# Kernel tuning notes

Measured on AMD Instinct MI355X. Metric: run time of the kernel, lower is better.

Reference implementation:

```python
import jax, jax.numpy as jnp
import numpy as np

# ---- Kymatio-style Morlet scattering filter bank (J=2, L=8, padded 40x40) ----
_CACHE = {}
_MP = 40  # 32 + 2*4 reflect padding, as in kymatio compute_padding for J=2

def _gabor(M, N, sigma, theta, xi, slant):
    R = np.array([[np.cos(theta), -np.sin(theta)], [np.sin(theta), np.cos(theta)]])
    D = np.array([[1.0, 0.0], [0.0, slant ** 2]])
    curv = R @ D @ R.T / (2.0 * sigma ** 2)
    xx, yy = np.mgrid[0:M, 0:N]
    gab = np.zeros((M, N), np.complex128)
    for ex in range(-2, 3):  # periodize over 5x5 shifts
        for ey in range(-2, 3):
            xg = xx + ex * M
            yg = yy + ey * N
            arg = -(curv[0, 0] * xg * xg + (curv[0, 1] + curv[1, 0]) * xg * yg + curv[1, 1] * yg * yg) \
                  + 1j * (xg * xi * np.cos(theta) + yg * xi * np.sin(theta))
            gab += np.exp(arg)
    return gab / (2.0 * np.pi * sigma ** 2 / slant)

def _morlet(M, N, sigma, theta, xi, slant):
    wv = _gabor(M, N, sigma, theta, xi, slant)
    env = _gabor(M, N, sigma, theta, 0.0, slant)
    return wv - (wv.sum() / env.sum()) * env  # zero-mean Morlet

def _periodize(v, res):
    k = 2 ** res
    Mv, Nv = v.shape
    return v.reshape(k, Mv // k, k, Nv // k).mean(axis=(0, 2))

def _filters():
    if _CACHE:
        return _CACHE
    Mp = _MP
    phi = np.real(np.fft.fft2(_gabor(Mp, Mp, 0.8 * 2 ** 2, 0.0, 0.0, 1.0)))
    psis = {}
    for j in range(2):
        bank = []
        for t in range(8):
            theta = (3 - t) * np.pi / 8.0  # kymatio angle convention (L=8)
            bank.append(np.real(np.fft.fft2(_morlet(Mp, Mp, 0.8 * 2 ** j, theta, 3.0 * np.pi / 4.0 / 2 ** j, 0.5))))
        psis[j] = np.stack(bank)
    _CACHE['phi0'] = jnp.asarray(phi, jnp.float32)
    _CACHE['phi1'] = jnp.asarray(_periodize(phi, 1), jnp.float32)
    _CACHE['psi0'] = jnp.asarray(psis[0], jnp.float32)      # (8,40,40) j=0 at res 0
    _CACHE['psi1_r0'] = jnp.asarray(psis[1], jnp.float32)   # (8,40,40) j=1 at res 0
    return _CACHE

def _unpad_sub(y_real, k):
    # fourier lowpass output -> spatial subsample by k, then unpad 1-pixel border
    return y_real[..., ::k, ::k][..., 1:-1, 1:-1]

def _scatter(x):
    F = _filters()
    xp = jnp.pad(x, ((0, 0), (0, 0), (4, 4), (4, 4)), mode='reflect')  # (B,3,40,40)
    xf = jnp.fft.fft2(xp)
    def lowpass(u, phi, k):
        return _unpad_sub(jnp.fft.ifft2(jnp.fft.fft2(u) * phi).real, k)
    # order 0
    S0 = _unpad_sub(jnp.fft.ifft2(xf * F['phi0']).real, 4)[:, :, None]            # (B,3,1,8,8)
    # order 1, j1 = 0 (stays at res 0)
    U1a = jnp.abs(jnp.fft.ifft2(xf[:, :, None] * F['psi0']))                       # (B,3,8,40,40)
    S1a = lowpass(U1a, F['phi0'], 4)                                               # (B,3,8,8,8)
    # order 1, j1 = 1 (subsample by 2)
    U1b = jnp.abs(jnp.fft.ifft2(xf[:, :, None] * F['psi1_r0'])[..., ::2, ::2])     # (B,3,8,20,20)
    S1b = lowpass(U1b, F['phi1'], 2)                                               # (B,3,8,8,8)
    # order 2, j1=0 -> j2=1
    U2 = jnp.abs(jnp.fft.ifft2(jnp.fft.fft2(U1a)[:, :, :, None] * F['psi1_r0'])[..., ::2, ::2])  # (B,3,8,8,20,20)
    S2 = lowpass(U2, F['phi1'], 2).reshape(x.shape[0], 3, 64, 8, 8)
    return jnp.concatenate([S0, S1a, S1b, S2], axis=2)  # (B,3,81,8,8)

def _toeplitz_mult(G, H, v):
    # ToeplitzLike, corner=False -> f=(0,0): y = sum_i L(g_i) (L(h_i)^T v)
    # L(.) lower-triangular Toeplitz; done via length-2n FFT conv / correlation
    n = v.shape[-1]
    Lf = 2 * n
    Hf = jnp.fft.rfft(H, Lf)          # (r, F)
    Gf = jnp.fft.rfft(G, Lf)          # (r, F)
    Vf = jnp.fft.rfft(v, Lf)          # (B, F)
    T = jnp.fft.irfft(jnp.conj(Hf)[:, None, :] * Vf[None], Lf)[..., :n]   # (r,B,n) = L(h_i)^T v
    Tf = jnp.fft.rfft(T, Lf)
    y = jnp.fft.irfft(jnp.einsum('rf,rbf->bf', Gf, Tf), Lf)[..., :n]       # sum_i L(g_i) t_i
    return y

def setup_inputs() -> dict:
    key = jax.random.key(0)
    ks = jax.random.split(key, 5)
    B, n, r = 128, 3 * 81 * 8 * 8, 4
    x = jax.random.normal(ks[0], (B, 3, 32, 32), jnp.float32)
    gamma = jnp.ones((n,), jnp.float32)
    beta = jnp.zeros((n,), jnp.float32)
    G = jax.random.normal(ks[3], (r, n), jnp.float32) / np.float32(np.sqrt(n))
    H = jax.random.normal(ks[4], (r, n), jnp.float32) / np.float32(np.sqrt(n))
    return {"x": x, "gamma": gamma, "beta": beta, "G": G, "H": H}

def reference(x, gamma, beta, G, H):
    S = _scatter(x)                                   # (B,3,81,8,8)
    f = S.reshape(S.shape[0], -1)                     # (B, 15552)
    mu = f.mean(axis=0)
    var = f.var(axis=0)                               # biased var, training-mode BN
    f = (f - mu) / jnp.sqrt(var + 1e-5) * gamma + beta
    f = jax.nn.relu(f)
    y = _toeplitz_mult(G, H, f)
    return y[..., :10]
```

## Files before the change

### kernel.cpp

```cpp
#include <hip/hip_runtime.h>
#include <math.h>

#define NTHR 256

__device__ __forceinline__ int reflect32(int v) {
  if (v < 0) v = -v;
  if (v > 31) v = 62 - v;
  return v;
}

__device__ __forceinline__ void init_tw(float2* tw, int N, int tid) {
  for (int j = tid; j < N; j += NTHR) {
    float s, c;
    sincosf(-2.0f * (float)M_PI * (float)j / (float)N, &s, &c);
    tw[j] = make_float2(c, s);
  }
}

template<int N, int LD, int NK, bool INV, int B, int AS>
__device__ __forceinline__ void dftB_rows(const float2* __restrict__ io,
                                          float2* __restrict__ tmp,
                                          const float2* __restrict__ tw, int tid) {
  constexpr int G = N / NK;
  constexpr int UNITS = B * N * G;
  for (int u = tid; u < UNITS; u += NTHR) {
    const int a = u / (N * G);
    const int rem = u - a * (N * G);
    const int r = rem / G, kg = rem - G * r;
    float xr[NK], xi[NK], ar[NK], ai[NK];
#pragma unroll
    for (int j = 0; j < NK; ++j) {
      float2 w = tw[kg * NK + j];
      xr[j] = w.x; xi[j] = INV ? -w.y : w.y;
    }
    const float2* row = io + a * AS + r * LD;
    float2 v = row[N - 1];
#pragma unroll
    for (int j = 0; j < NK; ++j) { ar[j] = v.x; ai[j] = v.y; }
#pragma unroll 2
    for (int cc = N - 2; cc >= 0; --cc) {
      v = row[cc];
#pragma unroll
      for (int j = 0; j < NK; ++j) {
        float nr = fmaf(ar[j], xr[j], fmaf(-ai[j], xi[j], v.x));
        float ni = fmaf(ar[j], xi[j], fmaf(ai[j], xr[j], v.y));
        ar[j] = nr; ai[j] = ni;
      }
    }
    float2* orow = tmp + a * AS + r * LD + kg * NK;
#pragma unroll
    for (int j = 0; j < NK; ++j) orow[j] = make_float2(ar[j], ai[j]);
  }
}

template<int N, int LD, int NK, bool INV, int B, int AS>
__device__ __forceinline__ void dftB_cols(const float2* __restrict__ tmp,
                                          float2* __restrict__ io,
                                          const float2* __restrict__ tw, int tid) {
  constexpr int G = N / NK;
  constexpr int UNITS = B * N * G;
  for (int u = tid; u < UNITS; u += NTHR) {
    const int a = u / (N * G);
    const int rem = u - a * (N * G);
    const int k1g = rem / N, k2 = rem - N * k1g;
    float xr[NK], xi[NK], ar[NK], ai[NK];
#pragma unroll
    for (int j = 0; j < NK; ++j) {
      float2 w = tw[k1g * NK + j];
      xr[j] = w.x; xi[j] = INV ? -w.y : w.y;
    }
    const float2* col = tmp + a * AS + k2;
    float2 v = col[(N - 1) * LD];
#pragma unroll
    for (int j = 0; j < NK; ++j) { ar[j] = v.x; ai[j] = v.y; }
#pragma unroll 2
    for (int r = N - 2; r >= 0; --r) {
      v = col[r * LD];
#pragma unroll
      for (int j = 0; j < NK; ++j) {
        float nr = fmaf(ar[j], xr[j], fmaf(-ai[j], xi[j], v.x));
        float ni = fmaf(ar[j], xi[j], fmaf(ai[j], xr[j], v.y));
        ar[j] = nr; ai[j] = ni;
      }
    }
    constexpr float scale = INV ? (1.f / (float)(N * N)) : 1.f;
#pragma unroll
    for (int j = 0; j < NK; ++j)
      io[a * AS + (k1g * NK + j) * LD + k2] = make_float2(ar[j] * scale, ai[j] * scale);
  }
}

template<int N, int LD, int NK, bool INV, int B, int AS>
__device__ __forceinline__ void dft2dB(float2* io, float2* tmp, const float2* tw, int tid) {
  dftB_rows<N, LD, NK, INV, B, AS>(io, tmp, tw, tid);
  __syncthreads();
  dftB_cols<N, LD, NK, INV, B, AS>(tmp, io, tw, tid);
  __syncthreads();
}

template<bool INV>
__device__ __forceinline__ void r40_rowsA(const float2* __restrict__ io, float2* __restrict__ T,
                                          const float2* __restrict__ tw, int tid) {
  if (tid < 200) {
    const int r = tid / 5, n2 = tid - 5 * r;
    const float2* base = io + r * 41 + n2;
    float xr[8], xi[8], ar[8], ai[8];
#pragma unroll
    for (int k1 = 0; k1 < 8; ++k1) {
      float2 w = tw[5 * k1];
      xr[k1] = w.x; xi[k1] = INV ? -w.y : w.y;
    }
    float2 v = base[35];
#pragma unroll
    for (int k1 = 0; k1 < 8; ++k1) { ar[k1] = v.x; ai[k1] = v.y; }
#pragma unroll
    for (int n1 = 6; n1 >= 0; --n1) {
      v = base[5 * n1];
#pragma unroll
      for (int k1 = 0; k1 < 8; ++k1) {
        float nr = fmaf(ar[k1], xr[k1], fmaf(-ai[k1], xi[k1], v.x));
        float ni = fmaf(ar[k1], xi[k1], fmaf(ai[k1], xr[k1], v.y));
        ar[k1] = nr; ai[k1] = ni;
      }
    }
    float2* o = T + r * 41 + n2 * 8;
#pragma unroll
    for (int k1 = 0; k1 < 8; ++k1) {
      float2 w = tw[n2 * k1];
      float wy = INV ? -w.y : w.y;
      o[k1] = make_float2(ar[k1] * w.x - ai[k1] * wy, ar[k1] * wy + ai[k1] * w.x);
    }
  }
}

template<bool INV>
__device__ __forceinline__ void r40_rowsB(const float2* __restrict__ T, float2* __restrict__ io,
                                          const float2* __restrict__ tw, int tid) {
  for (int u = tid; u < 320; u += NTHR) {
    const int r = u >> 3, k1 = u & 7;
    const float2* base = T + r * 41 + k1;
    float xr[5], xi[5], ar[5], ai[5];
#pragma unroll
    for (int k2 = 0; k2 < 5; ++k2) {
      float2 w = tw[8 * k2];
      xr[k2] = w.x; xi[k2] = INV ? -w.y : w.y;
    }
    float2 v = base[32];
#pragma unroll
    for (int k2 = 0; k2 < 5; ++k2) { ar[k2] = v.x; ai[k2] = v.y; }
#pragma unroll
    for (int n2 = 3; n2 >= 0; --n2) {
      v = base[n2 * 8];
#pragma unroll
      for (int k2 = 0; k2 < 5; ++k2) {
        float nr = fmaf(ar[k2], xr[k2], fmaf(-ai[k2], xi[k2], v.x));
        float ni = fmaf(ar[k2], xi[k2], fmaf(ai[k2], xr[k2], v.y));
        ar[k2] = nr; ai[k2] = ni;
      }
    }
    float2* o = io + r * 41 + k1;
#pragma unroll
    for (int k2 = 0; k2 < 5; ++k2) o[8 * k2] = make_float2(ar[k2], ai[k2]);
  }
}

template<bool INV>
__device__ __forceinline__ void r40_colsA(const float2* __restrict__ io, float2* __restrict__ T,
                                          const float2* __restrict__ tw, int tid) {
  if (tid < 200) {
    const int n2 = tid / 40, c = tid - 40 * n2;
    const float2* base = io + n2 * 41 + c;
    float xr[8], xi[8], ar[8], ai[8];
#pragma unroll
    for (int k1 = 0; k1 < 8; ++k1) {
      float2 w = tw[5 * k1];
      xr[k1] = w.x; xi[k1] = INV ? -w.y : w.y;
    }
    float2 v = base[35 * 41];
#pragma unroll
    for (int k1 = 0; k1 < 8; ++k1) { ar[k1] = v.x; ai[k1] = v.y; }
#pragma unroll
    for (int n1 = 6; n1 >= 0; --n1) {
      v = base[5 * n1 * 41];
#pragma unroll
      for (int k1 = 0; k1 < 8; ++k1) {
        float nr = fmaf(ar[k1], xr[k1], fmaf(-ai[k1], xi[k1], v.x));
        float ni = fmaf(ar[k1], xi[k1], fmaf(ai[k1], xr[k1], v.y));
        ar[k1] = nr; ai[k1] = ni;
      }
    }
    float2* o = T + n2 * 8 * 41 + c;
#pragma unroll
    for (int k1 = 0; k1 < 8; ++k1) {
      float2 w = tw[n2 * k1];
      float wy = INV ? -w.y : w.y;
      o[k1 * 41] = make_float2(ar[k1] * w.x - ai[k1] * wy, ar[k1] * wy + ai[k1] * w.x);
    }
  }
}

template<bool INV>
__device__ __forceinline__ void r40_colsB(const float2* __restrict__ T, float2* __restrict__ io,
                                          const float2* __restrict__ tw, int tid) {
  constexpr float scale = INV ? (1.f / 1600.f) : 1.f;
  for (int u = tid; u < 320; u += NTHR) {
    const int k1 = u / 40, c = u - 40 * k1;
    const float2* base = T + k1 * 41 + c;
    float xr[5], xi[5], ar[5], ai[5];
#pragma unroll
    for (int k2 = 0; k2 < 5; ++k2) {
      float2 w = tw[8 * k2];
      xr[k2] = w.x; xi[k2] = INV ? -w.y : w.y;
    }
    float2 v = base[4 * 8 * 41];
#pragma unroll
    for (int k2 = 0; k2 < 5; ++k2) { ar[k2] = v.x; ai[k2] = v.y; }
#pragma unroll
    for (int n2 = 3; n2 >= 0; --n2) {
      v = base[n2 * 8 * 41];
#pragma unroll
      for (int k2 = 0; k2 < 5; ++k2) {
        float nr = fmaf(ar[k2], xr[k2], fmaf(-ai[k2], xi[k2], v.x));
        float ni = fmaf(ar[k2], xi[k2], fmaf(ai[k2], xr[k2], v.y));
        ar[k2] = nr; ai[k2] = ni;
      }
    }
    float2* o = io + k1 * 41 + c;
#pragma unroll
    for (int k2 = 0; k2 < 5; ++k2)
      o[8 * k2 * 41] = make_float2(ar[k2] * scale, ai[k2] * scale);
  }
}

template<bool INV>
__device__ __forceinline__ void radix40(float2* io, float2* T, const float2* tw, int tid) {
  r40_rowsA<INV>(io, T, tw, tid);
  __syncthreads();
  r40_rowsB<INV>(T, io, tw, tid);
  __syncthreads();
  r40_colsA<INV>(io, T, tw, tid);
  __syncthreads();
  r40_colsB<INV>(T, io, tw, tid);
  __syncthreads();
}

__global__ __launch_bounds__(NTHR) void k_filters(float* __restrict__ filt) {
  const int fid = blockIdx.x;
  const int tid = threadIdx.x;

  __shared__ float2 WV[40 * 41];
  __shared__ float  EV[1600];
  __shared__ float2 T[40 * 41];
  __shared__ float2 tw40[40];
  __shared__ float  sred[3][4];
  __shared__ float  Kc[2];

  double sigma, theta, xi, slant; int morlet;
  if (fid == 0)      { sigma = 3.2; theta = 0.0; xi = 0.0;                  slant = 1.0; morlet = 0; }
  else if (fid <= 8) { int t = fid - 1; sigma = 0.8; theta = (3 - t) * M_PI / 8.0; xi = 3.0 * M_PI / 4.0; slant = 0.5; morlet = 1; }
  else               { int t = fid - 9; sigma = 1.6; theta = (3 - t) * M_PI / 8.0; xi = 3.0 * M_PI / 8.0; slant = 0.5; morlet = 1; }

  const double ctd = cos(theta), std_ = sin(theta);
  const double sl2 = slant * slant;
  const double inv2s = 1.0 / (2.0 * sigma * sigma);
  const float ca = (float)((ctd * ctd + sl2 * std_ * std_) * inv2s);
  const float cb = (float)((ctd * std_ * (1.0 - sl2)) * inv2s);
  const float cd = (float)((std_ * std_ + sl2 * ctd * ctd) * inv2s);
  const float rnorm = (float)(slant / (2.0 * M_PI * sigma * sigma));
  const float ct = (float)ctd, st = (float)std_;
  const float xif = (float)xi;

  float swr = 0.f, swi = 0.f, ser = 0.f;
  for (int o = tid; o < 1600; o += NTHR) {
    int xr = o / 40, yc = o - 40 * xr;
    float wr = 0.f, wi = 0.f, er = 0.f;
    for (int ex = -2; ex <= 2; ++ex) {
      for (int ey = -2; ey <= 2; ++ey) {
        float xg = (float)xr + ex * 40.f, yg = (float)yc + ey * 40.f;
        float e = expf(-(ca * xg * xg + 2.f * cb * xg * yg + cd * yg * yg));
        float ang = xif * (xg * ct + yg * st);
        float s, c;
        sincosf(ang, &s, &c);
        wr = fmaf(e, c, wr); wi = fmaf(e, s, wi); er += e;
      }
    }
    wr *= rnorm; wi *= rnorm; er *= rnorm;
    WV[xr * 41 + yc] = make_float2(wr, wi);
    EV[o] = er;
    swr += wr; swi += wi; ser += er;
  }
  for (int off = 32; off > 0; off >>= 1) {
    swr += __shfl_down(swr, off);
    swi += __shfl_down(swi, off);
    ser += __shfl_down(ser, off);
  }
  int lane = tid & 63, w = tid >> 6;
  if (lane == 0) { sred[0][w] = swr; sred[1][w] = swi; sred[2][w] = ser; }
  __syncthreads();
  if (tid == 0) {
    float A = 0, B = 0, C = 0;
    for (int i = 0; i < 4; ++i) { A += sred[0][i]; B += sred[1][i]; C += sred[2][i]; }
    Kc[0] = A / C; Kc[1] = B / C;
  }
  init_tw(tw40, 40, tid);
  __syncthreads();
  if (morlet) {
    for (int o = tid; o < 1600; o += NTHR) {
      int i = o / 40, j = o - 40 * i;
      float e = EV[o];
      WV[i * 41 + j].x -= Kc[0] * e;
      WV[i * 41 + j].y -= Kc[1] * e;
    }
  }
  __syncthreads();
  dft2dB<40, 41, 8, false, 1, 0>(WV, T, tw40, tid);

  if (fid == 0) {
    for (int o = tid; o < 1600; o += NTHR) {
      int q = o >> 4, j = o & 15;
      int q1 = q / 10, q2 = q - 10 * q1;
      int a2 = j >> 2, b2 = j & 3;
      filt[o] = WV[(q1 + 10 * a2) * 41 + (q2 + 10 * b2)].x * (1.f / 16.f);
    }
    for (int m = tid; m < 400; m += NTHR) {
      int m1 = m / 20, m2 = m - 20 * m1;
      EV[m] = 0.25f * (WV[m1 * 41 + m2].x + WV[(m1 + 20) * 41 + m2].x +
                       WV[m1 * 41 + m2 + 20].x + WV[(m1 + 20) * 41 + m2 + 20].x);
    }
    __syncthreads();
    for (int o = tid; o < 400; o += NTHR) {
      int q = o >> 2, j = o & 3;
      int q1 = q / 10, q2 = q - 10 * q1;
      int a2 = j >> 1, b2 = j & 1;
      filt[1600 + o] = EV[(q1 + 10 * a2) * 20 + (q2 + 10 * b2)] * 0.25f;
    }
  } else if (fid <= 8) {
    int t = fid - 1;
    for (int o = tid; o < 1600; o += NTHR) {
      int i = o / 40, j = o - 40 * i;
      filt[2000 + t * 1600 + o] = WV[i * 41 + j].x;
    }
  } else {
    int t = fid - 9;
    for (int q = tid; q < 400; q += NTHR) {
      int q1 = q / 20, q2 = q - 20 * q1;
      int base = q1 * 41 + q2;
      float* o = filt + 14800 + t * 1600 + q * 4;
      o[0] = WV[base].x * 0.25f;
      o[1] = WV[base + 20].x * 0.25f;
      o[2] = WV[base + 820].x * 0.25f;
      o[3] = WV[base + 840].x * 0.25f;
    }
  }
}

__global__ __launch_bounds__(NTHR) void k_fftx(const float* __restrict__ x,
                                               const float* __restrict__ filt,
                                               float2* __restrict__ xf_g,
                                               float* __restrict__ f) {
  const int bc = blockIdx.x;
  const int b = bc / 3, c = bc - 3 * b;
  const int tid = threadIdx.x;

  __shared__ float2 A[40 * 41], T[40 * 41];
  __shared__ float2 P[110];
  __shared__ float2 tw40[40], tw10[10];

  init_tw(tw40, 40, tid);
  init_tw(tw10, 10, tid);

  const float* xb = x + (size_t)bc * 1024;
  for (int o = tid; o < 1600; o += NTHR) {
    int i = o / 40, j = o - 40 * i;
    int si = reflect32(i - 4), sj = reflect32(j - 4);
    A[i * 41 + j] = make_float2(xb[si * 32 + sj], 0.f);
  }
  __syncthreads();
  radix40<false>(A, T, tw40, tid);
  for (int o = tid; o < 1600; o += NTHR) {
    int i = o / 40, j = o - 40 * i;
    xf_g[(size_t)bc * 1600 + o] = A[i * 41 + j];
  }

  const float4* ph0f4 = (const float4*)filt;
  for (int q = tid; q < 100; q += NTHR) {
    int q1 = q / 10, q2 = q - 10 * q1;
    int base = q1 * 41 + q2;
    float re = 0.f, im = 0.f;
#pragma unroll
    for (int a2 = 0; a2 < 4; ++a2) {
      float4 pf = ph0f4[q * 4 + a2];
      float2 v0 = A[base + a2 * 410];
      float2 v1 = A[base + a2 * 410 + 10];
      float2 v2 = A[base + a2 * 410 + 20];
      float2 v3 = A[base + a2 * 410 + 30];
      re = fmaf(v0.x, pf.x, fmaf(v1.x, pf.y, fmaf(v2.x, pf.z, fmaf(v3.x, pf.w, re))));
      im = fmaf(v0.y, pf.x, fmaf(v1.y, pf.y, fmaf(v2.y, pf.z, fmaf(v3.y, pf.w, im))));
    }
    P[q1 * 11 + q2] = make_float2(re, im);
  }
  __syncthreads();
  dft2dB<10, 11, 1, true, 1, 0>(P, T, tw10, tid);
  float* fb = f + (size_t)b * 15552 + c * 5184;
  if (tid < 64) {
    int i = tid >> 3, j = tid & 7;
    fb[tid] = P[(i + 1) * 11 + (j + 1)].x;
  }
}

__global__ __launch_bounds__(NTHR) void k_main(const float2* __restrict__ xf_g,
                                               const float* __restrict__ filt,
                                               float* __restrict__ f) {
  const int blk = blockIdx.x;
  const int t = blk & 7;
  const int bc = blk >> 3;
  const int b = bc / 3, c = bc - 3 * b;
  const int tid = threadIdx.x;

  __shared__ float2 A[40 * 41];
  __shared__ float2 T[40 * 41];
  __shared__ float2 C[2 * 420];
  __shared__ float2 P[110];
  __shared__ float2 P4[4 * 110];
  __shared__ float2 tw40[40], tw20[20], tw10[10];

  const float4* ph0f4 = (const float4*)filt;
  const float4* ph1f4 = (const float4*)(filt + 1600);
  const float*  psi0  = filt + 2000;
  const float4* ps1f4 = (const float4*)(filt + 14800);

  init_tw(tw40, 40, tid);
  init_tw(tw20, 20, tid);
  init_tw(tw10, 10, tid);

  const float2* xf = xf_g + (size_t)bc * 1600;
  for (int o = tid; o < 1600; o += NTHR) {
    int i = o / 40, j = o - 40 * i;
    A[i * 41 + j] = xf[o];
  }
  __syncthreads();

  float* fb = f + (size_t)b * 15552 + c * 5184;

  for (int q = tid; q < 400; q += NTHR) {
    int q1 = q / 20, q2 = q - 20 * q1;
    int base = q1 * 41 + q2;
    float4 pf = ps1f4[t * 400 + q];
    float2 v0 = A[base], v1 = A[base + 20], v2 = A[base + 820], v3 = A[base + 840];
    float re = fmaf(v0.x, pf.x, fmaf(v1.x, pf.y, fmaf(v2.x, pf.z, v3.x * pf.w)));
    float im = fmaf(v0.y, pf.x, fmaf(v1.y, pf.y, fmaf(v2.y, pf.z, v3.y * pf.w)));
    C[q1 * 21 + q2] = make_float2(re, im);
  }
  __syncthreads();
  dft2dB<20, 21, 2, true, 1, 420>(C, T, tw20, tid);
  for (int o = tid; o < 400; o += NTHR) {
    int i = o / 20, j = o - 20 * i;
    float2 z = C[i * 21 + j];
    C[i * 21 + j] = make_float2(sqrtf(fmaf(z.x, z.x, z.y * z.y)), 0.f);
  }
  __syncthreads();
  dft2dB<20, 21, 2, false, 1, 420>(C, T, tw20, tid);
  for (int q = tid; q < 100; q += NTHR) {
    int q1 = q / 10, q2 = q - 10 * q1;
    int base = q1 * 21 + q2;
    float4 pf = ph1f4[q];
    float2 v0 = C[base], v1 = C[base + 10], v2 = C[base + 210], v3 = C[base + 220];
    float re = fmaf(v0.x, pf.x, fmaf(v1.x, pf.y, fmaf(v2.x, pf.z, v3.x * pf.w)));
    float im = fmaf(v0.y, pf.x, fmaf(v1.y, pf.y, fmaf(v2.y, pf.z, v3.y * pf.w)));
    P[q1 * 11 + q2] = make_float2(-im, re);
  }

  const float* ps0 = psi0 + t * 1600;
  __syncthreads();
  for (int o = tid; o < 1600; o += NTHR) {
    int i = o / 40, j = o - 40 * i;
    float p = ps0[o];
    float2 v = A[i * 41 + j];
    A[i * 41 + j] = make_float2(v.x * p, v.y * p);
  }
  __syncthreads();
  radix40<true>(A, T, tw40, tid);
  for (int o = tid; o < 1600; o += NTHR) {
    int i = o / 40, j = o - 40 * i;
    float2 z = A[i * 41 + j];
    A[i * 41 + j] = make_float2(sqrtf(fmaf(z.x, z.x, z.y * z.y)), 0.f);
  }
  __syncthreads();
  radix40<false>(A, T, tw40, tid);

  for (int q = tid; q < 100; q += NTHR) {
    int q1 = q / 10, q2 = q - 10 * q1;
    int base = q1 * 41 + q2;
    float re = 0.f, im = 0.f;
#pragma unroll
    for (int a2 = 0; a2 < 4; ++a2) {
      float4 pf = ph0f4[q * 4 + a2];
      float2 v0 = A[base + a2 * 410];
      float2 v1 = A[base + a2 * 410 + 10];
      float2 v2 = A[base + a2 * 410 + 20];
      float2 v3 = A[base + a2 * 410 + 30];
      re = fmaf(v0.x, pf.x, fmaf(v1.x, pf.y, fmaf(v2.x, pf.z, fmaf(v3.x, pf.w, re))));
      im = fmaf(v0.y, pf.x, fmaf(v1.y, pf.y, fmaf(v2.y, pf.z, fmaf(v3.y, pf.w, im))));
    }
    float2 prev = P[q1 * 11 + q2];
    P[q1 * 11 + q2] = make_float2(prev.x + re, prev.y + im);
  }
  __syncthreads();
  dft2dB<10, 11, 1, true, 1, 0>(P, T, tw10, tid);
  if (tid < 64) {
    int i = tid >> 3, j = tid & 7;
    float2 v = P[(i + 1) * 11 + (j + 1)];
    fb[(1 + t) * 64 + tid] = v.x;
    fb[(9 + t) * 64 + tid] = v.y;
  }

  for (int p = 0; p < 4; ++p) {
    __syncthreads();
    for (int u = tid; u < 800; u += NTHR) {
      int a = (u >= 400) ? 1 : 0;
      int q = u - 400 * a;
      int q1 = q / 20, q2 = q - 20 * q1;
      int base = q1 * 41 + q2;
      float4 pf = ps1f4[(2 * p + a) * 400 + q];
      float2 v0 = A[base], v1 = A[base + 20], v2 = A[base + 820], v3 = A[base + 840];
      float re = fmaf(v0.x, pf.x, fmaf(v1.x, pf.y, fmaf(v2.x, pf.z, v3.x * pf.w)));
      float im = fmaf(v0.y, pf.x, fmaf(v1.y, pf.y, fmaf(v2.y, pf.z, v3.y * pf.w)));
      C[a * 420 + q1 * 21 + q2] = make_float2(re, im);
    }
    __syncthreads();
    dft2dB<20, 21, 2, true, 2, 420>(C, T, tw20, tid);
    for (int o = tid; o < 400; o += NTHR) {
      int i = o / 20, j = o - 20 * i;
      int idx = i * 21 + j;
      float2 z0 = C[idx], z1 = C[420 + idx];
      C[idx] = make_float2(sqrtf(fmaf(z0.x, z0.x, z0.y * z0.y)),
                           sqrtf(fmaf(z1.x, z1.x, z1.y * z1.y)));
    }
    __syncthreads();
    dft2dB<20, 21, 2, false, 1, 420>(C, T, tw20, tid);
    for (int q = tid; q < 100; q += NTHR) {
      int q1 = q / 10, q2 = q - 10 * q1;
      int base = q1 * 21 + q2;
      float4 pf = ph1f4[q];
      float2 v0 = C[base], v1 = C[base + 10], v2 = C[base + 210], v3 = C[base + 220];
      float re = fmaf(v0.x, pf.x, fmaf(v1.x, pf.y, fmaf(v2.x, pf.z, v3.x * pf.w)));
      float im = fmaf(v0.y, pf.x, fmaf(v1.y, pf.y, fmaf(v2.y, pf.z, v3.y * pf.w)));
      P4[p * 110 + q1 * 11 + q2] = make_float2(re, im);
    }
  }
  __syncthreads();
  dft2dB<10, 11, 1, true, 4, 110>(P4, T, tw10, tid);
  {
    int p = tid >> 6, o = tid & 63;
    int i = o >> 3, j = o & 7;
    float2 v = P4[p * 110 + (i + 1) * 11 + (j + 1)];
    fb[(17 + t * 8 + 2 * p) * 64 + o] = v.x;
    fb[(17 + t * 8 + 2 * p + 1) * 64 + o] = v.y;
  }
}

__global__ __launch_bounds__(NTHR) void k_bn(const float* __restrict__ f,
                                             float* __restrict__ mu,
                                             float* __restrict__ rstd) {
  int col = blockIdx.x * NTHR + threadIdx.x;
  if (col >= 15552) return;
  double s = 0.0, s2 = 0.0;
  for (int b = 0; b < 128; ++b) {
    float v = f[(size_t)b * 15552 + col];
    s += v; s2 += (double)v * v;
  }
  double m = s / 128.0;
  double var = s2 / 128.0 - m * m;
  mu[col] = (float)m;
  rstd[col] = (float)(1.0 / sqrt(var + 1e-5));
}

__global__ __launch_bounds__(NTHR) void k_out(const float* __restrict__ f,
                                              const float* __restrict__ mu,
                                              const float* __restrict__ rstd,
                                              const float* __restrict__ gamma,
                                              const float* __restrict__ beta,
                                              const float* __restrict__ Gm,
                                              const float* __restrict__ Hm,
                                              float* __restrict__ out) {
  const int b = blockIdx.x;
  const int tid = threadIdx.x;
  const float* fbp = f + (size_t)b * 15552;

  __shared__ float sg[NTHR + 10];
  float acc[40];
#pragma unroll
  for (int i = 0; i < 40; ++i) acc[i] = 0.f;

  for (int base = 0; base < 15552; base += NTHR) {
    int j = base + tid;
    float v = 0.f;
    if (j < 15552) {
      v = (fbp[j] - mu[j]) * rstd[j] * gamma[j] + beta[j];
      v = v > 0.f ? v : 0.f;
    }
    sg[tid] = v;
    if (tid < 10) {
      int j2 = base + NTHR + tid;
      float v2 = 0.f;
      if (j2 < 15552) {
        v2 = (fbp[j2] - mu[j2]) * rstd[j2] * gamma[j2] + beta[j2];
        v2 = v2 > 0.f ? v2 : 0.f;
      }
      sg[NTHR + tid] = v2;
    }
    __syncthreads();
    if (j < 15552) {
      float h[4];
#pragma unroll
      for (int r = 0; r < 4; ++r) h[r] = Hm[r * 15552 + j];
#pragma unroll
      for (int m = 0; m < 10; ++m) {
        float gv = sg[tid + m];
#pragma unroll
        for (int r = 0; r < 4; ++r) acc[r * 10 + m] = fmaf(h[r], gv, acc[r * 10 + m]);
      }
    }
    __syncthreads();
  }
#pragma unroll
  for (int i = 0; i < 40; ++i)
    for (int off = 32; off > 0; off >>= 1)
      acc[i] += __shfl_down(acc[i], off);

  __shared__ float red[4][40];
  __shared__ float Tm[40];
  int lane = tid & 63, w = tid >> 6;
  if (lane == 0) {
#pragma unroll
    for (int i = 0; i < 40; ++i) red[w][i] = acc[i];
  }
  __syncthreads();
  if (tid < 40) Tm[tid] = red[0][tid] + red[1][tid] + red[2][tid] + red[3][tid];
  __syncthreads();
  if (tid < 10) {
    float y = 0.f;
    for (int r = 0; r < 4; ++r)
      for (int m = 0; m <= tid; ++m)
        y += Gm[r * 15552 + (tid - m)] * Tm[r * 10 + m];
    out[b * 10 + tid] = y;
  }
}

extern "C" void kernel_launch(void* const* d_in, const int* in_sizes, int n_in,
                              void* d_out, int out_size, void* d_ws, size_t ws_size,
                              hipStream_t stream) {
  (void)in_sizes; (void)n_in; (void)out_size; (void)ws_size;
  const float* x     = (const float*)d_in[0];
  const float* gamma = (const float*)d_in[1];
  const float* beta  = (const float*)d_in[2];
  const float* G     = (const float*)d_in[3];
  const float* H     = (const float*)d_in[4];
  float* out = (float*)d_out;

  float* ws   = (float*)d_ws;
  float* filt = ws;
  float* xf   = filt + 27600;
  float* f    = xf + 1228800;
  float* mu   = f + 1990656;
  float* rstd = mu + 15552;

  k_filters<<<17, NTHR, 0, stream>>>(filt);
  k_fftx<<<384, NTHR, 0, stream>>>(x, filt, (float2*)xf, f);
  k_main<<<3072, NTHR, 0, stream>>>((const float2*)xf, filt, f);
  k_bn<<<61, NTHR, 0, stream>>>(f, mu, rstd);
  k_out<<<128, NTHR, 0, stream>>>(f, mu, rstd, gamma, beta, G, H, out);
}
```

Baseline: 382.1 us.

## Batch second-order paths with register FFT20, alias shared memory, prefetch BN loads

The second-order scattering stage now processes all 8 orientations at once instead of four pairs in a loop. It uses a register-resident radix-4x5 FFT20 in split real/imag layout and fuses the modulus into the forward row pass, packing two real signals into one complex FFT. Shared memory is aliased into one buffer, which cuts the footprint and may raise occupancy. Separately, k_bn unrolls its batch loads by 8, and k_out software-pipelines the normalize/ReLU loads for the next chunk. The cost is higher register pressure from 40-float register arrays, and only 160 or 80 threads are active during the FFT20 passes.

```diff
diff --git a/kernel.cpp b/kernel.cpp
--- a/kernel.cpp
+++ b/kernel.cpp
@@ -96,6 +96,113 @@
   __syncthreads();
   dftB_cols<N, LD, NK, INV, B, AS>(tmp, io, tw, tid);
   __syncthreads();
+}
+
+template<bool INV>
+__device__ __forceinline__ void fft20_reg(float* xr, float* xi) {
+  const float C20[13] = {1.f, 0.9510565162951535f, 0.8090169943749475f, 0.5877852522924731f,
+                         0.3090169943749474f, 0.f, -0.3090169943749474f, -0.5877852522924731f,
+                         -0.8090169943749475f, -0.9510565162951535f, -1.f, -0.9510565162951535f,
+                         -0.8090169943749475f};
+  const float S20[13] = {0.f, 0.3090169943749474f, 0.5877852522924731f, 0.8090169943749475f,
+                         0.9510565162951535f, 1.f, 0.9510565162951535f, 0.8090169943749475f,
+                         0.5877852522924731f, 0.3090169943749474f, 0.f, -0.3090169943749474f,
+                         -0.5877852522924731f};
+  float ur[20], ui[20];
+#pragma unroll
+  for (int n2 = 0; n2 < 5; ++n2) {
+    float x0r = xr[n2],      x0i = xi[n2];
+    float x1r = xr[5 + n2],  x1i = xi[5 + n2];
+    float x2r = xr[10 + n2], x2i = xi[10 + n2];
+    float x3r = xr[15 + n2], x3i = xi[15 + n2];
+    float e0r = x0r + x2r, e0i = x0i + x2i;
+    float d0r = x0r - x2r, d0i = x0i - x2i;
+    float e1r = x1r + x3r, e1i = x1i + x3i;
+    float d1r = x1r - x3r, d1i = x1i - x3i;
+    float y0r = e0r + e1r, y0i = e0i + e1i;
+    float y2r = e0r - e1r, y2i = e0i - e1i;
+    float y1r, y1i, y3r, y3i;
+    if (INV) { y1r = d0r - d1i; y1i = d0i + d1r; y3r = d0r + d1i; y3i = d0i - d1r; }
+    else     { y1r = d0r + d1i; y1i = d0i - d1r; y3r = d0r - d1i; y3i = d0i + d1r; }
+    ur[n2 * 4 + 0] = y0r; ui[n2 * 4 + 0] = y0i;
+    {
+      float c = C20[n2], s = INV ? S20[n2] : -S20[n2];
+      ur[n2 * 4 + 1] = y1r * c - y1i * s; ui[n2 * 4 + 1] = y1r * s + y1i * c;
+    }
+    {
+      float c = C20[2 * n2], s = INV ? S20[2 * n2] : -S20[2 * n2];
+      ur[n2 * 4 + 2] = y2r * c - y2i * s; ui[n2 * 4 + 2] = y2r * s + y2i * c;
+    }
+    {
+      float c = C20[3 * n2], s = INV ? S20[3 * n2] : -S20[3 * n2];
+      ur[n2 * 4 + 3] = y3r * c - y3i * s; ui[n2 * 4 + 3] = y3r * s + y3i * c;
+    }
+  }
+  const float C5[5] = {1.f, 0.3090169943749474f, -0.8090169943749475f, -0.8090169943749475f,
+                       0.3090169943749474f};
+  const float S5[5] = {0.f, 0.9510565162951535f, 0.5877852522924731f, -0.5877852522924731f,
+                       -0.9510565162951535f};
+#pragma unroll
+  for (int k1 = 0; k1 < 4; ++k1) {
+    float t0r = ur[k1],      t0i = ui[k1];
+    float t1r = ur[4 + k1],  t1i = ui[4 + k1];
+    float t2r = ur[8 + k1],  t2i = ui[8 + k1];
+    float t3r = ur[12 + k1], t3i = ui[12 + k1];
+    float t4r = ur[16 + k1], t4i = ui[16 + k1];
+#pragma unroll
+    for (int k2 = 0; k2 < 5; ++k2) {
+      float ar = t0r, ai = t0i;
+      { const int j = (1 * k2) % 5; float c = C5[j], s = INV ? S5[j] : -S5[j];
+        ar += t1r * c - t1i * s; ai += t1r * s + t1i * c; }
+      { const int j = (2 * k2) % 5; float c = C5[j], s = INV ? S5[j] : -S5[j];
+        ar += t2r * c - t2i * s; ai += t2r * s + t2i * c; }
+      { const int j = (3 * k2) % 5; float c = C5[j], s = INV ? S5[j] : -S5[j];
+        ar += t3r * c - t3i * s; ai += t3r * s + t3i * c; }
+      { const int j = (4 * k2) % 5; float c = C5[j], s = INV ? S5[j] : -S5[j];
+        ar += t4r * c - t4i * s; ai += t4r * s + t4i * c; }
+      xr[k1 + 4 * k2] = ar; xi[k1 + 4 * k2] = ai;
+    }
+  }
+}
+
+template<bool INV, int BATCH, bool SCALE, bool COLS>
+__device__ __forceinline__ void fused20_pass(float* __restrict__ UR, float* __restrict__ UI, int tid) {
+  if (tid < BATCH * 20) {
+    const int a = tid / 20, q = tid % 20;
+    const int off = a * 420 + (COLS ? q : q * 21);
+    const int st = COLS ? 21 : 1;
+    float xr[20], xi[20];
+#pragma unroll
+    for (int n = 0; n < 20; ++n) { xr[n] = UR[off + st * n]; xi[n] = UI[off + st * n]; }
+    fft20_reg<INV>(xr, xi);
+#pragma unroll
+    for (int n = 0; n < 20; ++n) {
+      float vr = xr[n], vi = xi[n];
+      if (SCALE) { vr *= (1.f / 400.f); vi *= (1.f / 400.f); }
+      UR[off + st * n] = vr; UI[off + st * n] = vi;
+    }
+  }
+}
+
+__device__ __forceinline__ void fwd20_rows_mag(const float* __restrict__ CR, const float* __restrict__ CI,
+                                               float* __restrict__ FR, float* __restrict__ FI, int tid) {
+  if (tid < 80) {
+    const int p = tid / 20, r = tid % 20;
+    const int i0 = (2 * p) * 420 + r * 21;
+    const int i1 = (2 * p + 1) * 420 + r * 21;
+    float xr[20], xi[20];
+#pragma unroll
+    for (int n = 0; n < 20; ++n) {
+      float a0 = CR[i0 + n], b0 = CI[i0 + n];
+      float a1 = CR[i1 + n], b1 = CI[i1 + n];
+      xr[n] = sqrtf(fmaf(a0, a0, b0 * b0));
+      xi[n] = sqrtf(fmaf(a1, a1, b1 * b1));
+    }
+    fft20_reg<false>(xr, xi);
+    const int off = p * 420 + r * 21;
+#pragma unroll
+    for (int n = 0; n < 20; ++n) { FR[off + n] = xr[n]; FI[off + n] = xi[n]; }
+  }
 }
 
 template<bool INV>
@@ -417,12 +524,22 @@
   const int b = bc / 3, c = bc - 3 * b;
   const int tid = threadIdx.x;
 
-  __shared__ float2 A[40 * 41];
-  __shared__ float2 T[40 * 41];
-  __shared__ float2 C[2 * 420];
-  __shared__ float2 P[110];
-  __shared__ float2 P4[4 * 110];
-  __shared__ float2 tw40[40], tw20[20], tw10[10];
+  __shared__ float U[10220];
+  float2* A    = (float2*)U;
+  float*  FR   = U;
+  float*  FI   = U + 1680;
+  float*  CR   = U + 3360;
+  float*  CI   = U + 6720;
+  float2* C20  = (float2*)(U + 3360);
+  float2* T20  = (float2*)(U + 4200);
+  float2* T40  = (float2*)(U + 3360);
+  float2* P    = (float2*)(U + 6700);
+  float2* SC1  = (float2*)(U + 7000);
+  float2* P4   = (float2*)(U + 3360);
+  float2* SC4  = (float2*)(U + 4400);
+  float2* tw40 = (float2*)(U + 10080);
+  float2* tw20 = (float2*)(U + 10160);
+  float2* tw10 = (float2*)(U + 10200);
 
   const float4* ph0f4 = (const float4*)filt;
   const float4* ph1f4 = (const float4*)(filt + 1600);
@@ -449,22 +566,22 @@
     float2 v0 = A[base], v1 = A[base + 20], v2 = A[base + 820], v3 = A[base + 840];
     float re = fmaf(v0.x, pf.x, fmaf(v1.x, pf.y, fmaf(v2.x, pf.z, v3.x * pf.w)));
     float im = fmaf(v0.y, pf.x, fmaf(v1.y, pf.y, fmaf(v2.y, pf.z, v3.y * pf.w)));
-    C[q1 * 21 + q2] = make_float2(re, im);
-  }
-  __syncthreads();
-  dft2dB<20, 21, 2, true, 1, 420>(C, T, tw20, tid);
+    C20[q1 * 21 + q2] = make_float2(re, im);
+  }
+  __syncthreads();
+  dft2dB<20, 21, 2, true, 1, 420>(C20, T20, tw20, tid);
   for (int o = tid; o < 400; o += NTHR) {
     int i = o / 20, j = o - 20 * i;
-    float2 z = C[i * 21 + j];
-    C[i * 21 + j] = make_float2(sqrtf(fmaf(z.x, z.x, z.y * z.y)), 0.f);
-  }
-  __syncthreads();
-  dft2dB<20, 21, 2, false, 1, 420>(C, T, tw20, tid);
+    float2 z = C20[i * 21 + j];
+    C20[i * 21 + j] = make_float2(sqrtf(fmaf(z.x, z.x, z.y * z.y)), 0.f);
+  }
+  __syncthreads();
+  dft2dB<20, 21, 2, false, 1, 420>(C20, T20, tw20, tid);
   for (int q = tid; q < 100; q += NTHR) {
     int q1 = q / 10, q2 = q - 10 * q1;
     int base = q1 * 21 + q2;
     float4 pf = ph1f4[q];
-    float2 v0 = C[base], v1 = C[base + 10], v2 = C[base + 210], v3 = C[base + 220];
+    float2 v0 = C20[base], v1 = C20[base + 10], v2 = C20[base + 210], v3 = C20[base + 220];
     float re = fmaf(v0.x, pf.x, fmaf(v1.x, pf.y, fmaf(v2.x, pf.z, v3.x * pf.w)));
     float im = fmaf(v0.y, pf.x, fmaf(v1.y, pf.y, fmaf(v2.y, pf.z, v3.y * pf.w)));
     P[q1 * 11 + q2] = make_float2(-im, re);
@@ -479,14 +596,14 @@
     A[i * 41 + j] = make_float2(v.x * p, v.y * p);
   }
   __syncthreads();
-  radix40<true>(A, T, tw40, tid);
+  radix40<true>(A, T40, tw40, tid);
   for (int o = tid; o < 1600; o += NTHR) {
     int i = o / 40, j = o - 40 * i;
     float2 z = A[i * 41 + j];
     A[i * 41 + j] = make_float2(sqrtf(fmaf(z.x, z.x, z.y * z.y)), 0.f);
   }
   __syncthreads();
-  radix40<false>(A, T, tw40, tid);
+  radix40<false>(A, T40, tw40, tid);
 
   for (int q = tid; q < 100; q += NTHR) {
     int q1 = q / 10, q2 = q - 10 * q1;
@@ -506,50 +623,48 @@
     P[q1 * 11 + q2] = make_float2(prev.x + re, prev.y + im);
   }
   __syncthreads();
-  dft2dB<10, 11, 1, true, 1, 0>(P, T, tw10, tid);
+  dft2dB<10, 11, 1, true, 1, 0>(P, SC1, tw10, tid);
   if (tid < 64) {
     int i = tid >> 3, j = tid & 7;
     float2 v = P[(i + 1) * 11 + (j + 1)];
     fb[(1 + t) * 64 + tid] = v.x;
     fb[(9 + t) * 64 + tid] = v.y;
   }
-
-  for (int p = 0; p < 4; ++p) {
-    __syncthreads();
-    for (int u = tid; u < 800; u += NTHR) {
-      int a = (u >= 400) ? 1 : 0;
-      int q = u - 400 * a;
-      int q1 = q / 20, q2 = q - 20 * q1;
-      int base = q1 * 41 + q2;
-      float4 pf = ps1f4[(2 * p + a) * 400 + q];
-      float2 v0 = A[base], v1 = A[base + 20], v2 = A[base + 820], v3 = A[base + 840];
-      float re = fmaf(v0.x, pf.x, fmaf(v1.x, pf.y, fmaf(v2.x, pf.z, v3.x * pf.w)));
-      float im = fmaf(v0.y, pf.x, fmaf(v1.y, pf.y, fmaf(v2.y, pf.z, v3.y * pf.w)));
-      C[a * 420 + q1 * 21 + q2] = make_float2(re, im);
-    }
-    __syncthreads();
-    dft2dB<20, 21, 2, true, 2, 420>(C, T, tw20, tid);
-    for (int o = tid; o < 400; o += NTHR) {
-      int i = o / 20, j = o - 20 * i;
-      int idx = i * 21 + j;
-      float2 z0 = C[idx], z1 = C[420 + idx];
-      C[idx] = make_float2(sqrtf(fmaf(z0.x, z0.x, z0.y * z0.y)),
-                           sqrtf(fmaf(z1.x, z1.x, z1.y * z1.y)));
-    }
-    __syncthreads();
-    dft2dB<20, 21, 2, false, 1, 420>(C, T, tw20, tid);
-    for (int q = tid; q < 100; q += NTHR) {
-      int q1 = q / 10, q2 = q - 10 * q1;
-      int base = q1 * 21 + q2;
-      float4 pf = ph1f4[q];
-      float2 v0 = C[base], v1 = C[base + 10], v2 = C[base + 210], v3 = C[base + 220];
-      float re = fmaf(v0.x, pf.x, fmaf(v1.x, pf.y, fmaf(v2.x, pf.z, v3.x * pf.w)));
-      float im = fmaf(v0.y, pf.x, fmaf(v1.y, pf.y, fmaf(v2.y, pf.z, v3.y * pf.w)));
-      P4[p * 110 + q1 * 11 + q2] = make_float2(re, im);
-    }
-  }
-  __syncthreads();
-  dft2dB<10, 11, 1, true, 4, 110>(P4, T, tw10, tid);
+  __syncthreads();
+
+  for (int u = tid; u < 3200; u += NTHR) {
+    int ch = u / 400, q = u - 400 * ch;
+    int q1 = q / 20, q2 = q - 20 * q1;
+    int base = q1 * 41 + q2;
+    float4 pf = ps1f4[ch * 400 + q];
+    float2 v0 = A[base], v1 = A[base + 20], v2 = A[base + 820], v3 = A[base + 840];
+    float re = fmaf(v0.x, pf.x, fmaf(v1.x, pf.y, fmaf(v2.x, pf.z, v3.x * pf.w)));
+    float im = fmaf(v0.y, pf.x, fmaf(v1.y, pf.y, fmaf(v2.y, pf.z, v3.y * pf.w)));
+    int o = ch * 420 + q1 * 21 + q2;
+    CR[o] = re; CI[o] = im;
+  }
+  __syncthreads();
+  fused20_pass<true, 8, false, false>(CR, CI, tid);
+  __syncthreads();
+  fused20_pass<true, 8, true, true>(CR, CI, tid);
+  __syncthreads();
+  fwd20_rows_mag(CR, CI, FR, FI, tid);
+  __syncthreads();
+  fused20_pass<false, 4, false, true>(FR, FI, tid);
+  __syncthreads();
+  for (int u = tid; u < 400; u += NTHR) {
+    int p = u / 100, q = u - 100 * p;
+    int q1 = q / 10, q2 = q - 10 * q1;
+    int base = p * 420 + q1 * 21 + q2;
+    float4 pf = ph1f4[q];
+    float re = fmaf(FR[base], pf.x, fmaf(FR[base + 10], pf.y,
+               fmaf(FR[base + 210], pf.z, FR[base + 220] * pf.w)));
+    float im = fmaf(FI[base], pf.x, fmaf(FI[base + 10], pf.y,
+               fmaf(FI[base + 210], pf.z, FI[base + 220] * pf.w)));
+    P4[p * 110 + q1 * 11 + q2] = make_float2(re, im);
+  }
+  __syncthreads();
+  dft2dB<10, 11, 1, true, 4, 110>(P4, SC4, tw10, tid);
   {
     int p = tid >> 6, o = tid & 63;
     int i = o >> 3, j = o & 7;
@@ -565,9 +680,12 @@
   int col = blockIdx.x * NTHR + threadIdx.x;
   if (col >= 15552) return;
   double s = 0.0, s2 = 0.0;
-  for (int b = 0; b < 128; ++b) {
-    float v = f[(size_t)b * 15552 + col];
-    s += v; s2 += (double)v * v;
+  for (int b = 0; b < 128; b += 8) {
+    float v[8];
+#pragma unroll
+    for (int u = 0; u < 8; ++u) v[u] = f[(size_t)(b + u) * 15552 + col];
+#pragma unroll
+    for (int u = 0; u < 8; ++u) { s += v[u]; s2 += (double)v[u] * v[u]; }
   }
   double m = s / 128.0;
   double var = s2 / 128.0 - m * m;
@@ -592,24 +710,38 @@
 #pragma unroll
   for (int i = 0; i < 40; ++i) acc[i] = 0.f;
 
+  float vcur, vtail = 0.f;
+  {
+    int j = tid;
+    float v = (fbp[j] - mu[j]) * rstd[j] * gamma[j] + beta[j];
+    vcur = v > 0.f ? v : 0.f;
+    if (tid < 10) {
+      int j2 = NTHR + tid;
+      float v2 = (fbp[j2] - mu[j2]) * rstd[j2] * gamma[j2] + beta[j2];
+      vtail = v2 > 0.f ? v2 : 0.f;
+    }
+  }
   for (int base = 0; base < 15552; base += NTHR) {
+    sg[tid] = vcur;
+    if (tid < 10) sg[NTHR + tid] = vtail;
+    __syncthreads();
+    float vnext = 0.f, vtn = 0.f;
+    int nbase = base + NTHR;
+    if (nbase < 15552) {
+      int j = nbase + tid;
+      if (j < 15552) {
+        float v = (fbp[j] - mu[j]) * rstd[j] * gamma[j] + beta[j];
+        vnext = v > 0.f ? v : 0.f;
+      }
+      if (tid < 10) {
+        int j2 = nbase + NTHR + tid;
+        if (j2 < 15552) {
+          float v2 = (fbp[j2] - mu[j2]) * rstd[j2] * gamma[j2] + beta[j2];
+          vtn = v2 > 0.f ? v2 : 0.f;
+        }
+      }
+    }
     int j = base + tid;
-    float v = 0.f;
-    if (j < 15552) {
-      v = (fbp[j] - mu[j]) * rstd[j] * gamma[j] + beta[j];
-      v = v > 0.f ? v : 0.f;
-    }
-    sg[tid] = v;
-    if (tid < 10) {
-      int j2 = base + NTHR + tid;
-      float v2 = 0.f;
-      if (j2 < 15552) {
-        v2 = (fbp[j2] - mu[j2]) * rstd[j2] * gamma[j2] + beta[j2];
-        v2 = v2 > 0.f ? v2 : 0.f;
-      }
-      sg[NTHR + tid] = v2;
-    }
-    __syncthreads();
     if (j < 15552) {
       float h[4];
 #pragma unroll
@@ -622,6 +754,7 @@
       }
     }
     __syncthreads();
+    vcur = vnext; vtail = vtn;
   }
 #pragma unroll
   for (int i = 0; i < 40; ++i)
```

Result: faster. 335.2 us (-12.3%).
